# Kernel optimization log

Hardware: AMD Instinct MI355X
Metric: run time of the kernel (lower is better)

Reference implementation:

```python
import jax, jax.numpy as jnp
import numpy as np

N = 65536   # total goals in library
D = 256     # flattened embedding dim
B = 2048    # batch_size (last B entries are the new batch)


def setup_inputs() -> dict:
    key = jax.random.key(0)
    k1, k2 = jax.random.split(key)
    return {
        "target_lib": jax.random.normal(k1, (N, D), dtype=jnp.float32),
        "reached_lib": jax.random.normal(k2, (N, D), dtype=jnp.float32),
        "batch_size": B,
    }


def _euclid(a, b):
    # distance_fn: Euclidean distance between two embeddings
    return jnp.sqrt(jnp.sum((a - b) ** 2))


def _nearest_idx(queries, lib):
    # top-1 nearest neighbor via squared-distance expansion (same argmin as cdist)
    qn = jnp.sum(queries * queries, axis=1, keepdims=True)      # [B,1]
    ln = jnp.sum(lib * lib, axis=1)                             # [L]
    d2 = qn + ln[None, :] - 2.0 * (queries @ lib.T)             # [B,L]
    return jnp.argmin(d2, axis=1)                               # [B]


def reference(target_lib, reached_lib, batch_size):
    targets = target_lib[-batch_size:]          # [B,D] newest target goals
    reached = reached_lib[-batch_size:]         # [B,D] newest reached goals
    prev = reached_lib[:-batch_size]            # [N-B,D] previously reached goals

    prev_closest = prev[_nearest_idx(targets, prev)]       # [B,D]
    new_closest = reached[_nearest_idx(targets, reached)]  # [B,D]

    def LP(t, init_e, reached_e):
        return _euclid(t, init_e) - _euclid(t, reached_e)

    IM_vals, IM_grads = jax.vmap(jax.value_and_grad(LP, 0))(
        targets, prev_closest, new_closest)
    return IM_vals, IM_grads
```

## Files before the change

### kernel.cpp

```cpp
#include <hip/hip_runtime.h>
#include <math.h>

#define NTOT   65536
#define DDIM   256
#define BATCH  2048
#define NPREV  (NTOT - BATCH)

#define NC_P 31
#define CHUNK_P 2048
#define NC_R 16
#define CHUNK_R 128

#define INF_F 3.402823466e+38f
#define SWZ(r) ((((r) & 3)) ^ ((((r) >> 2) & 3)))

typedef float  f32x4  __attribute__((ext_vector_type(4)));
typedef float  f32x16 __attribute__((ext_vector_type(16)));
typedef _Float16 half8 __attribute__((ext_vector_type(8)));

#define TILE_HALVES 65536
#define KB_HALVES   8192

#define SCHED_FENCE() __builtin_amdgcn_sched_barrier(0)
#define RAW_BARRIER() do { SCHED_FENCE(); __builtin_amdgcn_s_barrier(); SCHED_FENCE(); } while (0)
#define VMCNT8()  do { asm volatile("s_waitcnt vmcnt(8)" ::: "memory"); SCHED_FENCE(); } while (0)
#define VMCNT0()  do { asm volatile("s_waitcnt vmcnt(0)" ::: "memory"); SCHED_FENCE(); } while (0)

__global__ void lp_norms(const float* __restrict__ lib, float* __restrict__ ln) {
    const int row  = blockIdx.x * 4 + (threadIdx.x >> 6);
    const int lane = threadIdx.x & 63;
    const float4 v = reinterpret_cast<const float4*>(lib + (size_t)row * DDIM)[lane];
    float s = v.x * v.x + v.y * v.y + v.z * v.z + v.w * v.w;
#pragma unroll
    for (int off = 32; off > 0; off >>= 1) s += __shfl_down(s, off);
    if (lane == 0) ln[row] = s;
}

__device__ __forceinline__ void cvt_split(const f32x4 a, const f32x4 b,
                                          half8& h, half8& l) {
    float v[8] = {a[0], a[1], a[2], a[3], b[0], b[1], b[2], b[3]};
#pragma unroll
    for (int j = 0; j < 8; ++j) {
        const float s = v[j] * 256.0f;
        const _Float16 hh = (_Float16)s;
        const _Float16 ll = (_Float16)(s - (float)hh);
        h[j] = hh; l[j] = ll;
    }
}

__global__ void lp_split32(const float* __restrict__ src, _Float16* __restrict__ dst,
                           float* __restrict__ ln) {
    const int tile = blockIdx.x;
    const int t    = threadIdx.x;
    const int rg   = t >> 6;
    const int l    = t & 63;
    const int row  = rg * 32 + (l & 31);
    const int k8   = l >> 5;
    const float* srcR = src + (size_t)tile * 128 * DDIM + (size_t)row * DDIM;
    _Float16*    dstT = dst + (size_t)tile * TILE_HALVES;

    float nsum = 0.f;
#pragma unroll
    for (int kb = 0; kb < 8; ++kb) {
#pragma unroll
        for (int kk = 0; kk < 2; ++kk) {
            const float* p = srcR + kb * 32 + kk * 16 + k8 * 8;
            const f32x4 a = *reinterpret_cast<const f32x4*>(p);
            const f32x4 b = *reinterpret_cast<const f32x4*>(p + 4);
            half8 h, lo; cvt_split(a, b, h, lo);
            const size_t off = ((size_t)(((kb * 2 + 0) * 4 + rg) * 2 + kk) * 64 + l) * 8;
            *reinterpret_cast<half8*>(dstT + off)        = h;
            *reinterpret_cast<half8*>(dstT + off + 4096) = lo;
            nsum += a[0]*a[0] + a[1]*a[1] + a[2]*a[2] + a[3]*a[3]
                  + b[0]*b[0] + b[1]*b[1] + b[2]*b[2] + b[3]*b[3];
        }
    }
    nsum += __shfl_xor(nsum, 32);
    if (ln != nullptr && k8 == 0) ln[(size_t)tile * 128 + row] = nsum;
}

__device__ __forceinline__ void stage4k(_Float16* lds, const _Float16* g, int t) {
    const int wid = t >> 6;
    __builtin_amdgcn_global_load_lds(
        (const __attribute__((address_space(1))) void*)(g + (size_t)t * 8),
        (__attribute__((address_space(3))) void*)(lds + (size_t)wid * 512),
        16, 0, 0);
}

__global__ __launch_bounds__(256, 2)
void lp_nn_mfma5(const _Float16* __restrict__ Qs, const _Float16* __restrict__ Ls,
                 const float* __restrict__ ln, int chunkRows,
                 float* __restrict__ pscore, int* __restrict__ pidx, int nchunks)
{
    __shared__ _Float16 B0[16384];
    __shared__ _Float16 B1[16384];
    __shared__ float xk[2][128];
    __shared__ int   xi[2][128];

    const int nwg  = 16 * nchunks;
    const int hid  = blockIdx.x;
    const int work = (hid & 7) * (nwg >> 3) + (hid >> 3);
    const int bx   = work & 15;
    const int by   = work >> 4;

    const int t    = threadIdx.x;
    const int wid  = t >> 6, lane = t & 63;
    const int wq   = wid >> 1, wl = wid & 1;
    const int col  = lane & 31, hi = lane >> 5;
    const int chunkBase = by * chunkRows;

    const _Float16* Qtile = Qs + (size_t)bx * TILE_HALVES;
    const _Float16* Lbase = Ls + (size_t)(chunkBase >> 7) * TILE_HALVES;
    const int NSTEP = (chunkRows >> 7) * 8;

    float bkey[2][16];
    int   bidxr[2][16];
    f32x16 acc[2][2];
#pragma unroll
    for (int mf = 0; mf < 2; ++mf) {
#pragma unroll
        for (int r = 0; r < 16; ++r) { bkey[mf][r] = INF_F; bidxr[mf][r] = 0x7fffffff; }
#pragma unroll
        for (int nf = 0; nf < 2; ++nf) acc[mf][nf] = (f32x16)(0.f);
    }

    auto stage = [&](_Float16* dst, int s) {
        const int kb = s & 7, lt = s >> 3;
        const _Float16* Qkb = Qtile + kb * KB_HALVES;
        const _Float16* Lkb = Lbase + (size_t)lt * TILE_HALVES + kb * KB_HALVES;
#pragma unroll
        for (int i = 0; i < 4; ++i) stage4k(dst + i * 2048,        Qkb + i * 2048, t);
#pragma unroll
        for (int i = 0; i < 4; ++i) stage4k(dst + 8192 + i * 2048, Lkb + i * 2048, t);
    };

    auto compute = [&](const _Float16* buf, int s) {
        const _Float16* Ab = buf;
        const _Float16* Bb = buf + 8192;
#pragma unroll
        for (int kk = 0; kk < 2; ++kk) {
            half8 a[2][2], b[2][2];
#pragma unroll
            for (int mf = 0; mf < 2; ++mf)
#pragma unroll
                for (int hl = 0; hl < 2; ++hl) {
                    a[mf][hl] = *reinterpret_cast<const half8*>(
                        Ab + (((hl * 4 + (wq * 2 + mf)) * 2 + kk) * 64 + lane) * 8);
                    b[mf][hl] = *reinterpret_cast<const half8*>(
                        Bb + (((hl * 4 + (wl * 2 + mf)) * 2 + kk) * 64 + lane) * 8);
                }
#pragma unroll
            for (int nf = 0; nf < 2; ++nf)
#pragma unroll
                for (int mf = 0; mf < 2; ++mf) {
                    acc[mf][nf] = __builtin_amdgcn_mfma_f32_32x32x16_f16(a[mf][0], b[nf][0], acc[mf][nf], 0, 0, 0);
                    acc[mf][nf] = __builtin_amdgcn_mfma_f32_32x32x16_f16(a[mf][0], b[nf][1], acc[mf][nf], 0, 0, 0);
                    acc[mf][nf] = __builtin_amdgcn_mfma_f32_32x32x16_f16(a[mf][1], b[nf][0], acc[mf][nf], 0, 0, 0);
                }
        }
        if ((s & 7) == 7) {
            const int ltbase = chunkBase + ((s >> 3) << 7);
#pragma unroll
            for (int nf = 0; nf < 2; ++nf) {
                const int gidx = ltbase + wl * 64 + nf * 32 + col;
                const float lnv = ln[gidx] * 65536.0f;
#pragma unroll
                for (int mf = 0; mf < 2; ++mf)
#pragma unroll
                    for (int r = 0; r < 16; ++r) {
                        const float key = fmaf(-2.f, acc[mf][nf][r], lnv);
                        if (key < bkey[mf][r] || (key == bkey[mf][r] && gidx < bidxr[mf][r])) {
                            bkey[mf][r] = key; bidxr[mf][r] = gidx;
                        }
                        acc[mf][nf][r] = 0.f;
                    }
            }
        }
    };

    stage(B0, 0);
    for (int s = 0; s < NSTEP; s += 2) {
        stage(B1, s + 1);
        VMCNT8();
        RAW_BARRIER();
        compute(B0, s);
        RAW_BARRIER();
        if (s + 2 < NSTEP) { stage(B0, s + 2); VMCNT8(); }
        else               { VMCNT0(); }
        RAW_BARRIER();
        compute(B1, s + 1);
        RAW_BARRIER();
    }

#pragma unroll
    for (int off = 1; off < 32; off <<= 1) {
#pragma unroll
        for (int mf = 0; mf < 2; ++mf)
#pragma unroll
            for (int r = 0; r < 16; ++r) {
                const float ok = __shfl_xor(bkey[mf][r], off);
                const int   oi = __shfl_xor(bidxr[mf][r], off);
                if (ok < bkey[mf][r] || (ok == bkey[mf][r] && oi < bidxr[mf][r])) {
                    bkey[mf][r] = ok; bidxr[mf][r] = oi;
                }
            }
    }
    if (col == 0) {
#pragma unroll
        for (int mf = 0; mf < 2; ++mf)
#pragma unroll
            for (int r = 0; r < 16; ++r) {
                const int ql = wq * 64 + mf * 32 + (r & 3) + 8 * (r >> 2) + 4 * hi;
                xk[wl][ql] = bkey[mf][r];
                xi[wl][ql] = bidxr[mf][r];
            }
    }
    __syncthreads();
    if (t < 128) {
        float bk = xk[0][t]; int bi = xi[0][t];
        const float k2 = xk[1][t]; const int i2 = xi[1][t];
        if (k2 < bk || (k2 == bk && i2 < bi)) { bk = k2; bi = i2; }
        const int q = bx * 128 + t;
        pscore[(size_t)q * nchunks + by] = bk;
        pidx  [(size_t)q * nchunks + by] = bi;
    }
}

__global__ __launch_bounds__(256, 2)
void lp_nn_mfma_fb(const float* __restrict__ Q, const float* __restrict__ L,
                   const float* __restrict__ ln, int chunkRows,
                   float* __restrict__ pscore, int* __restrict__ pidx, int nchunks)
{
    __shared__ _Float16 Ah[128 * 32];
    __shared__ _Float16 Al[128 * 32];
    __shared__ _Float16 Bh[128 * 32];
    __shared__ _Float16 Bl[128 * 32];
    __shared__ float xk[2][128];
    __shared__ int   xi[2][128];

    const int t    = threadIdx.x;
    const int wid  = t >> 6, lane = t & 63;
    const int wq   = wid >> 1, wl = wid & 1;
    const int col  = lane & 15, rg = lane >> 4;
    const int qbase = blockIdx.x * 128;
    const int chunkBase = blockIdx.y * chunkRows;
    const int srow   = t >> 2;
    const int schunk = t & 3;

    float bkey[4][4];
    int   bidxr[4][4];
#pragma unroll
    for (int mf = 0; mf < 4; ++mf)
#pragma unroll
        for (int i = 0; i < 4; ++i) { bkey[mf][i] = INF_F; bidxr[mf][i] = 0x7fffffff; }

    for (int lt = 0; lt < chunkRows; lt += 128) {
        f32x4 acc[4][4];
#pragma unroll
        for (int mf = 0; mf < 4; ++mf)
#pragma unroll
            for (int nf = 0; nf < 4; ++nf) acc[mf][nf] = (f32x4)(0.f);

        for (int kb = 0; kb < DDIM; kb += 32) {
            __syncthreads();
#pragma unroll
            for (int sr = 0; sr < 2; ++sr) {
                const int r = srow + 64 * sr;
                const int s = schunk ^ SWZ(r);
                {
                    const float* src = Q + (size_t)(qbase + r) * DDIM + kb + schunk * 8;
                    const f32x4 a = *reinterpret_cast<const f32x4*>(src);
                    const f32x4 b = *reinterpret_cast<const f32x4*>(src + 4);
                    half8 h, l; cvt_split(a, b, h, l);
                    *reinterpret_cast<half8*>(&Ah[r * 32 + s * 8]) = h;
                    *reinterpret_cast<half8*>(&Al[r * 32 + s * 8]) = l;
                }
                {
                    const float* src = L + (size_t)(chunkBase + lt + r) * DDIM + kb + schunk * 8;
                    const f32x4 a = *reinterpret_cast<const f32x4*>(src);
                    const f32x4 b = *reinterpret_cast<const f32x4*>(src + 4);
                    half8 h, l; cvt_split(a, b, h, l);
                    *reinterpret_cast<half8*>(&Bh[r * 32 + s * 8]) = h;
                    *reinterpret_cast<half8*>(&Bl[r * 32 + s * 8]) = l;
                }
            }
            __syncthreads();

            half8 ah[4], al[4];
#pragma unroll
            for (int mf = 0; mf < 4; ++mf) {
                const int r = wq * 64 + mf * 16 + col;
                const int s = rg ^ SWZ(r);
                ah[mf] = *reinterpret_cast<const half8*>(&Ah[r * 32 + s * 8]);
                al[mf] = *reinterpret_cast<const half8*>(&Al[r * 32 + s * 8]);
            }
#pragma unroll
            for (int nf = 0; nf < 4; ++nf) {
                const int r = wl * 64 + nf * 16 + col;
                const int s = rg ^ SWZ(r);
                const half8 bh = *reinterpret_cast<const half8*>(&Bh[r * 32 + s * 8]);
                const half8 bl = *reinterpret_cast<const half8*>(&Bl[r * 32 + s * 8]);
#pragma unroll
                for (int mf = 0; mf < 4; ++mf) {
                    acc[mf][nf] = __builtin_amdgcn_mfma_f32_16x16x32_f16(ah[mf], bh, acc[mf][nf], 0, 0, 0);
                    acc[mf][nf] = __builtin_amdgcn_mfma_f32_16x16x32_f16(ah[mf], bl, acc[mf][nf], 0, 0, 0);
                    acc[mf][nf] = __builtin_amdgcn_mfma_f32_16x16x32_f16(al[mf], bh, acc[mf][nf], 0, 0, 0);
                }
            }
        }

#pragma unroll
        for (int nf = 0; nf < 4; ++nf) {
            const int gidx = chunkBase + lt + wl * 64 + nf * 16 + col;
            const float lnv = ln[gidx] * 65536.0f;
#pragma unroll
            for (int mf = 0; mf < 4; ++mf)
#pragma unroll
                for (int i = 0; i < 4; ++i) {
                    const float key = fmaf(-2.f, acc[mf][nf][i], lnv);
                    if (key < bkey[mf][i] || (key == bkey[mf][i] && gidx < bidxr[mf][i])) {
                        bkey[mf][i] = key; bidxr[mf][i] = gidx;
                    }
                }
        }
    }

#pragma unroll
    for (int off = 1; off < 16; off <<= 1) {
#pragma unroll
        for (int mf = 0; mf < 4; ++mf)
#pragma unroll
            for (int i = 0; i < 4; ++i) {
                const float ok = __shfl_xor(bkey[mf][i], off);
                const int   oi = __shfl_xor(bidxr[mf][i], off);
                if (ok < bkey[mf][i] || (ok == bkey[mf][i] && oi < bidxr[mf][i])) {
                    bkey[mf][i] = ok; bidxr[mf][i] = oi;
                }
            }
    }
    if (col == 0) {
#pragma unroll
        for (int mf = 0; mf < 4; ++mf)
#pragma unroll
            for (int i = 0; i < 4; ++i) {
                const int ql = wq * 64 + mf * 16 + rg * 4 + i;
                xk[wl][ql] = bkey[mf][i];
                xi[wl][ql] = bidxr[mf][i];
            }
    }
    __syncthreads();
    if (t < 128) {
        float bk = xk[0][t]; int bi = xi[0][t];
        const float k2 = xk[1][t]; const int i2 = xi[1][t];
        if (k2 < bk || (k2 == bk && i2 < bi)) { bk = k2; bi = i2; }
        const int q = qbase + t;
        pscore[(size_t)q * nchunks + blockIdx.y] = bk;
        pidx  [(size_t)q * nchunks + blockIdx.y] = bi;
    }
}

__global__ void lp_finalize(const float* __restrict__ Q,
                            const float* __restrict__ prevL,
                            const float* __restrict__ reachL,
                            const float* __restrict__ ps_p, const int* __restrict__ pi_p,
                            const float* __restrict__ ps_r, const int* __restrict__ pi_r,
                            float* __restrict__ out)
{
    const int q = blockIdx.x;
    const int lane = threadIdx.x;

    float k1 = (lane < NC_P) ? ps_p[(size_t)q * NC_P + lane] : INF_F;
    int   i1 = (lane < NC_P) ? pi_p[(size_t)q * NC_P + lane] : 0x7fffffff;
#pragma unroll
    for (int off = 32; off > 0; off >>= 1) {
        const float ok = __shfl_xor(k1, off);
        const int   oi = __shfl_xor(i1, off);
        if (ok < k1 || (ok == k1 && oi < i1)) { k1 = ok; i1 = oi; }
    }
    float k2 = (lane < NC_R) ? ps_r[(size_t)q * NC_R + lane] : INF_F;
    int   i2 = (lane < NC_R) ? pi_r[(size_t)q * NC_R + lane] : 0x7fffffff;
#pragma unroll
    for (int off = 32; off > 0; off >>= 1) {
        const float ok = __shfl_xor(k2, off);
        const int   oi = __shfl_xor(i2, off);
        if (ok < k2 || (ok == k2 && oi < i2)) { k2 = ok; i2 = oi; }
    }

    const float4 tv = reinterpret_cast<const float4*>(Q      + (size_t)q  * DDIM)[lane];
    const float4 e1 = reinterpret_cast<const float4*>(prevL  + (size_t)i1 * DDIM)[lane];
    const float4 e2 = reinterpret_cast<const float4*>(reachL + (size_t)i2 * DDIM)[lane];
    const float4 d1 = {tv.x - e1.x, tv.y - e1.y, tv.z - e1.z, tv.w - e1.w};
    const float4 d2 = {tv.x - e2.x, tv.y - e2.y, tv.z - e2.z, tv.w - e2.w};
    float s1 = d1.x * d1.x + d1.y * d1.y + d1.z * d1.z + d1.w * d1.w;
    float s2 = d2.x * d2.x + d2.y * d2.y + d2.z * d2.z + d2.w * d2.w;
#pragma unroll
    for (int off = 32; off > 0; off >>= 1) {
        s1 += __shfl_xor(s1, off);
        s2 += __shfl_xor(s2, off);
    }
    const float r1 = sqrtf(s1), r2 = sqrtf(s2);
    float4 g;
    g.x = d1.x / r1 - d2.x / r2;
    g.y = d1.y / r1 - d2.y / r2;
    g.z = d1.z / r1 - d2.z / r2;
    g.w = d1.w / r1 - d2.w / r2;
    reinterpret_cast<float4*>(out + BATCH + (size_t)q * DDIM)[lane] = g;
    if (lane == 0) out[q] = r1 - r2;
}

extern "C" void kernel_launch(void* const* d_in, const int* in_sizes, int n_in,
                              void* d_out, int out_size, void* d_ws, size_t ws_size,
                              hipStream_t stream) {
    const float* target_lib  = (const float*)d_in[0];
    const float* reached_lib = (const float*)d_in[1];
    const float* Qp     = target_lib  + (size_t)NPREV * DDIM;
    const float* prevL  = reached_lib;
    const float* reachL = reached_lib + (size_t)NPREV * DDIM;

    float* ws     = (float*)d_ws;
    float* ln_all = ws;
    float* ps_p   = ln_all + NTOT;
    float* ps_r   = ps_p + (size_t)BATCH * NC_P;
    int*   pi_p   = (int*)(ps_r + (size_t)BATCH * NC_R);
    int*   pi_r   = pi_p + (size_t)BATCH * NC_P;
    _Float16* Qsp = (_Float16*)(pi_r + (size_t)BATCH * NC_R);
    _Float16* Lsp = Qsp + (size_t)(BATCH / 128) * TILE_HALVES;
    float* out    = (float*)d_out;

    const size_t need = 1032192u
                      + (size_t)(BATCH / 128) * TILE_HALVES * 2
                      + (size_t)(NTOT / 128) * TILE_HALVES * 2;

    if (ws_size >= need) {
        lp_split32<<<NTOT / 128, 256, 0, stream>>>(reached_lib, Lsp, ln_all);
        lp_split32<<<BATCH / 128, 256, 0, stream>>>(Qp, Qsp, nullptr);
        lp_nn_mfma5<<<16 * NC_P, 256, 0, stream>>>(
            Qsp, Lsp, ln_all, CHUNK_P, ps_p, pi_p, NC_P);
        lp_nn_mfma5<<<16 * NC_R, 256, 0, stream>>>(
            Qsp, Lsp + (size_t)(NPREV / 128) * TILE_HALVES,
            ln_all + NPREV, CHUNK_R, ps_r, pi_r, NC_R);
    } else {
        lp_norms<<<NTOT / 4, 256, 0, stream>>>(reached_lib, ln_all);
        lp_nn_mfma_fb<<<dim3(BATCH / 128, NC_P), 256, 0, stream>>>(
            Qp, prevL, ln_all, CHUNK_P, ps_p, pi_p, NC_P);
        lp_nn_mfma_fb<<<dim3(BATCH / 128, NC_R), 256, 0, stream>>>(
            Qp, reachL, ln_all + NPREV, CHUNK_R, ps_r, pi_r, NC_R);
    }
    lp_finalize<<<BATCH, 64, 0, stream>>>(Qp, prevL, reachL, ps_p, pi_p, ps_r, pi_r, out);
}
```

Measured before the change: 278.5 us.

## Widen NN kernel to 256-query tiles with 8 waves and staged norms

Replaces the 256-thread 128x128 MFMA nearest-neighbor kernel with a 512-thread variant in which each workgroup covers 256 queries against 128 library rows per step. Library tiles are now reused across twice as many queries. Library norms are preloaded into LDS, and the next stage is issued after compute within each step. LDS fragment loads are split around the MFMA groups with barriers and setprio hints. The reached-chunk split changes to 8 chunks of 256 rows. The cost is more LDS per workgroup and more barriers per step, which may reduce occupancy.

```diff
diff --git a/kernel.cpp b/kernel.cpp
--- a/kernel.cpp
+++ b/kernel.cpp
@@ -8,8 +8,8 @@
 
 #define NC_P 31
 #define CHUNK_P 2048
-#define NC_R 16
-#define CHUNK_R 128
+#define NC_R 8
+#define CHUNK_R 256
 
 #define INF_F 3.402823466e+38f
 #define SWZ(r) ((((r) & 3)) ^ ((((r) >> 2) & 3)))
@@ -23,8 +23,9 @@
 
 #define SCHED_FENCE() __builtin_amdgcn_sched_barrier(0)
 #define RAW_BARRIER() do { SCHED_FENCE(); __builtin_amdgcn_s_barrier(); SCHED_FENCE(); } while (0)
-#define VMCNT8()  do { asm volatile("s_waitcnt vmcnt(8)" ::: "memory"); SCHED_FENCE(); } while (0)
+#define VMCNT6()  do { asm volatile("s_waitcnt vmcnt(6)" ::: "memory"); SCHED_FENCE(); } while (0)
 #define VMCNT0()  do { asm volatile("s_waitcnt vmcnt(0)" ::: "memory"); SCHED_FENCE(); } while (0)
+#define LGKM0()   do { asm volatile("s_waitcnt lgkmcnt(0)" ::: "memory"); SCHED_FENCE(); } while (0)
 
 __global__ void lp_norms(const float* __restrict__ lib, float* __restrict__ ln) {
     const int row  = blockIdx.x * 4 + (threadIdx.x >> 6);
@@ -79,39 +80,51 @@
     if (ln != nullptr && k8 == 0) ln[(size_t)tile * 128 + row] = nsum;
 }
 
-__device__ __forceinline__ void stage4k(_Float16* lds, const _Float16* g, int t) {
-    const int wid = t >> 6;
+__device__ __forceinline__ void stage8(_Float16* lds, const _Float16* g, int t) {
     __builtin_amdgcn_global_load_lds(
         (const __attribute__((address_space(1))) void*)(g + (size_t)t * 8),
-        (__attribute__((address_space(3))) void*)(lds + (size_t)wid * 512),
+        (__attribute__((address_space(3))) void*)(lds + (size_t)(t >> 6) * 512),
         16, 0, 0);
 }
 
-__global__ __launch_bounds__(256, 2)
-void lp_nn_mfma5(const _Float16* __restrict__ Qs, const _Float16* __restrict__ Ls,
+__global__ __launch_bounds__(512, 2)
+void lp_nn_mfma6(const _Float16* __restrict__ Qs, const _Float16* __restrict__ Ls,
                  const float* __restrict__ ln, int chunkRows,
                  float* __restrict__ pscore, int* __restrict__ pidx, int nchunks)
 {
-    __shared__ _Float16 B0[16384];
-    __shared__ _Float16 B1[16384];
-    __shared__ float xk[2][128];
-    __shared__ int   xi[2][128];
-
-    const int nwg  = 16 * nchunks;
+    __shared__ _Float16 B0[24576];
+    __shared__ _Float16 B1[24576];
+    __shared__ float lnLds[2048];
+    __shared__ float xk[2][256];
+    __shared__ int   xi[2][256];
+
+    const int nwg  = 8 * nchunks;
     const int hid  = blockIdx.x;
     const int work = (hid & 7) * (nwg >> 3) + (hid >> 3);
-    const int bx   = work & 15;
-    const int by   = work >> 4;
+    const int bx   = work & 7;
+    const int by   = work >> 3;
 
     const int t    = threadIdx.x;
-    const int wid  = t >> 6, lane = t & 63;
-    const int wq   = wid >> 1, wl = wid & 1;
+    const int lane = t & 63;
+    const int wid  = t >> 6;
+    const int wq   = wid >> 1;
+    const int wl   = wid & 1;
     const int col  = lane & 31, hi = lane >> 5;
     const int chunkBase = by * chunkRows;
 
-    const _Float16* Qtile = Qs + (size_t)bx * TILE_HALVES;
+    const _Float16* Qt    = Qs + (size_t)(bx * 2) * TILE_HALVES;
     const _Float16* Lbase = Ls + (size_t)(chunkBase >> 7) * TILE_HALVES;
     const int NSTEP = (chunkRows >> 7) * 8;
+
+    int aB[2], bB[2];
+#pragma unroll
+    for (int mf = 0; mf < 2; ++mf) {
+        const int ql = wq * 64 + mf * 32;
+        aB[mf] = (ql >> 7) * 8192 + ((ql >> 5) & 3) * 1024 + lane * 8;
+    }
+#pragma unroll
+    for (int nf = 0; nf < 2; ++nf)
+        bB[nf] = 16384 + (wl * 2 + nf) * 1024 + lane * 8;
 
     float bkey[2][16];
     int   bidxr[2][16];
@@ -126,74 +139,90 @@
 
     auto stage = [&](_Float16* dst, int s) {
         const int kb = s & 7, lt = s >> 3;
-        const _Float16* Qkb = Qtile + kb * KB_HALVES;
+        const _Float16* Q0  = Qt + kb * KB_HALVES;
+        const _Float16* Q1  = Qt + TILE_HALVES + kb * KB_HALVES;
         const _Float16* Lkb = Lbase + (size_t)lt * TILE_HALVES + kb * KB_HALVES;
-#pragma unroll
-        for (int i = 0; i < 4; ++i) stage4k(dst + i * 2048,        Qkb + i * 2048, t);
-#pragma unroll
-        for (int i = 0; i < 4; ++i) stage4k(dst + 8192 + i * 2048, Lkb + i * 2048, t);
+        stage8(dst + 0,     Q0 + 0,    t);
+        stage8(dst + 4096,  Q0 + 4096, t);
+        stage8(dst + 8192,  Q1 + 0,    t);
+        stage8(dst + 12288, Q1 + 4096, t);
+        stage8(dst + 16384, Lkb + 0,    t);
+        stage8(dst + 20480, Lkb + 4096, t);
     };
 
-    auto compute = [&](const _Float16* buf, int s) {
-        const _Float16* Ab = buf;
-        const _Float16* Bb = buf + 8192;
-#pragma unroll
-        for (int kk = 0; kk < 2; ++kk) {
-            half8 a[2][2], b[2][2];
+    auto fold = [&](int lt) {
+#pragma unroll
+        for (int nf = 0; nf < 2; ++nf) {
+            const int lrow = lt * 128 + wl * 64 + nf * 32 + col;
+            const float lnv = lnLds[lrow] * 65536.0f;
+            const int gidx = chunkBase + lrow;
 #pragma unroll
             for (int mf = 0; mf < 2; ++mf)
 #pragma unroll
-                for (int hl = 0; hl < 2; ++hl) {
-                    a[mf][hl] = *reinterpret_cast<const half8*>(
-                        Ab + (((hl * 4 + (wq * 2 + mf)) * 2 + kk) * 64 + lane) * 8);
-                    b[mf][hl] = *reinterpret_cast<const half8*>(
-                        Bb + (((hl * 4 + (wl * 2 + mf)) * 2 + kk) * 64 + lane) * 8);
-                }
-#pragma unroll
-            for (int nf = 0; nf < 2; ++nf)
-#pragma unroll
-                for (int mf = 0; mf < 2; ++mf) {
-                    acc[mf][nf] = __builtin_amdgcn_mfma_f32_32x32x16_f16(a[mf][0], b[nf][0], acc[mf][nf], 0, 0, 0);
-                    acc[mf][nf] = __builtin_amdgcn_mfma_f32_32x32x16_f16(a[mf][0], b[nf][1], acc[mf][nf], 0, 0, 0);
-                    acc[mf][nf] = __builtin_amdgcn_mfma_f32_32x32x16_f16(a[mf][1], b[nf][0], acc[mf][nf], 0, 0, 0);
-                }
-        }
-        if ((s & 7) == 7) {
-            const int ltbase = chunkBase + ((s >> 3) << 7);
-#pragma unroll
-            for (int nf = 0; nf < 2; ++nf) {
-                const int gidx = ltbase + wl * 64 + nf * 32 + col;
-                const float lnv = ln[gidx] * 65536.0f;
-#pragma unroll
-                for (int mf = 0; mf < 2; ++mf)
-#pragma unroll
-                    for (int r = 0; r < 16; ++r) {
-                        const float key = fmaf(-2.f, acc[mf][nf][r], lnv);
-                        if (key < bkey[mf][r] || (key == bkey[mf][r] && gidx < bidxr[mf][r])) {
-                            bkey[mf][r] = key; bidxr[mf][r] = gidx;
-                        }
-                        acc[mf][nf][r] = 0.f;
+                for (int r = 0; r < 16; ++r) {
+                    const float key = fmaf(-2.f, acc[mf][nf][r], lnv);
+                    if (key < bkey[mf][r] || (key == bkey[mf][r] && gidx < bidxr[mf][r])) {
+                        bkey[mf][r] = key; bidxr[mf][r] = gidx;
                     }
-            }
+                    acc[mf][nf][r] = 0.f;
+                }
         }
     };
 
+    auto step = [&](_Float16* buf, int s) {
+        if (s + 1 < NSTEP) VMCNT6(); else VMCNT0();
+        RAW_BARRIER();
+        half8 a[2][2], bb[2];
+#pragma unroll
+        for (int kk = 0; kk < 2; ++kk) {
+#pragma unroll
+            for (int mf = 0; mf < 2; ++mf)
+#pragma unroll
+                for (int hl = 0; hl < 2; ++hl)
+                    a[mf][hl] = *reinterpret_cast<const half8*>(buf + aB[mf] + hl * 4096 + kk * 512);
+#pragma unroll
+            for (int hl = 0; hl < 2; ++hl)
+                bb[hl] = *reinterpret_cast<const half8*>(buf + bB[0] + hl * 4096 + kk * 512);
+            RAW_BARRIER(); LGKM0();
+            __builtin_amdgcn_s_setprio(1);
+#pragma unroll
+            for (int mf = 0; mf < 2; ++mf) {
+                acc[mf][0] = __builtin_amdgcn_mfma_f32_32x32x16_f16(a[mf][0], bb[0], acc[mf][0], 0, 0, 0);
+                acc[mf][0] = __builtin_amdgcn_mfma_f32_32x32x16_f16(a[mf][0], bb[1], acc[mf][0], 0, 0, 0);
+                acc[mf][0] = __builtin_amdgcn_mfma_f32_32x32x16_f16(a[mf][1], bb[0], acc[mf][0], 0, 0, 0);
+            }
+            __builtin_amdgcn_s_setprio(0);
+#pragma unroll
+            for (int hl = 0; hl < 2; ++hl)
+                bb[hl] = *reinterpret_cast<const half8*>(buf + bB[1] + hl * 4096 + kk * 512);
+            RAW_BARRIER(); LGKM0();
+            __builtin_amdgcn_s_setprio(1);
+#pragma unroll
+            for (int mf = 0; mf < 2; ++mf) {
+                acc[mf][1] = __builtin_amdgcn_mfma_f32_32x32x16_f16(a[mf][0], bb[0], acc[mf][1], 0, 0, 0);
+                acc[mf][1] = __builtin_amdgcn_mfma_f32_32x32x16_f16(a[mf][0], bb[1], acc[mf][1], 0, 0, 0);
+                acc[mf][1] = __builtin_amdgcn_mfma_f32_32x32x16_f16(a[mf][1], bb[0], acc[mf][1], 0, 0, 0);
+            }
+            __builtin_amdgcn_s_setprio(0);
+        }
+        RAW_BARRIER();
+        if (s + 2 < NSTEP) stage(buf, s + 2);
+        if ((s & 7) == 7) fold(s >> 3);
+    };
+
+    for (int i = t; i < chunkRows; i += 512) lnLds[i] = ln[chunkBase + i];
+    SCHED_FENCE();
     stage(B0, 0);
+    stage(B1, 1);
+    LGKM0();
+
     for (int s = 0; s < NSTEP; s += 2) {
-        stage(B1, s + 1);
-        VMCNT8();
-        RAW_BARRIER();
-        compute(B0, s);
-        RAW_BARRIER();
-        if (s + 2 < NSTEP) { stage(B0, s + 2); VMCNT8(); }
-        else               { VMCNT0(); }
-        RAW_BARRIER();
-        compute(B1, s + 1);
-        RAW_BARRIER();
-    }
-
-#pragma unroll
-    for (int off = 1; off < 32; off <<= 1) {
+        step(B0, s);
+        step(B1, s + 1);
+    }
+
+#pragma unroll
+    for (int off = 1; off < 32; off <<= 1)
 #pragma unroll
         for (int mf = 0; mf < 2; ++mf)
 #pragma unroll
@@ -204,8 +233,7 @@
                     bkey[mf][r] = ok; bidxr[mf][r] = oi;
                 }
             }
-    }
-    if (col == 0) {
+    if (col == 0)
 #pragma unroll
         for (int mf = 0; mf < 2; ++mf)
 #pragma unroll
@@ -214,13 +242,12 @@
                 xk[wl][ql] = bkey[mf][r];
                 xi[wl][ql] = bidxr[mf][r];
             }
-    }
     __syncthreads();
-    if (t < 128) {
+    if (t < 256) {
         float bk = xk[0][t]; int bi = xi[0][t];
         const float k2 = xk[1][t]; const int i2 = xi[1][t];
         if (k2 < bk || (k2 == bk && i2 < bi)) { bk = k2; bi = i2; }
-        const int q = bx * 128 + t;
+        const int q = bx * 256 + t;
         pscore[(size_t)q * nchunks + by] = bk;
         pidx  [(size_t)q * nchunks + by] = bi;
     }
@@ -326,7 +353,7 @@
     }
 
 #pragma unroll
-    for (int off = 1; off < 16; off <<= 1) {
+    for (int off = 1; off < 16; off <<= 1)
 #pragma unroll
         for (int mf = 0; mf < 4; ++mf)
 #pragma unroll
@@ -337,8 +364,7 @@
                     bkey[mf][i] = ok; bidxr[mf][i] = oi;
                 }
             }
-    }
-    if (col == 0) {
+    if (col == 0)
 #pragma unroll
         for (int mf = 0; mf < 4; ++mf)
 #pragma unroll
@@ -347,7 +373,6 @@
                 xk[wl][ql] = bkey[mf][i];
                 xi[wl][ql] = bidxr[mf][i];
             }
-    }
     __syncthreads();
     if (t < 128) {
         float bk = xk[0][t]; int bi = xi[0][t];
@@ -427,16 +452,15 @@
     _Float16* Lsp = Qsp + (size_t)(BATCH / 128) * TILE_HALVES;
     float* out    = (float*)d_out;
 
-    const size_t need = 1032192u
-                      + (size_t)(BATCH / 128) * TILE_HALVES * 2
-                      + (size_t)(NTOT / 128) * TILE_HALVES * 2;
+    const size_t need = (size_t)(NTOT + 2 * BATCH * (NC_P + NC_R)) * 4
+                      + (size_t)(BATCH / 128 + NTOT / 128) * TILE_HALVES * 2;
 
     if (ws_size >= need) {
         lp_split32<<<NTOT / 128, 256, 0, stream>>>(reached_lib, Lsp, ln_all);
         lp_split32<<<BATCH / 128, 256, 0, stream>>>(Qp, Qsp, nullptr);
-        lp_nn_mfma5<<<16 * NC_P, 256, 0, stream>>>(
+        lp_nn_mfma6<<<8 * NC_P, 512, 0, stream>>>(
             Qsp, Lsp, ln_all, CHUNK_P, ps_p, pi_p, NC_P);
-        lp_nn_mfma5<<<16 * NC_R, 256, 0, stream>>>(
+        lp_nn_mfma6<<<8 * NC_R, 512, 0, stream>>>(
             Qsp, Lsp + (size_t)(NPREV / 128) * TILE_HALVES,
             ln_all + NPREV, CHUNK_R, ps_r, pi_r, NC_R);
     } else {
```

New measurement: 301.2 us. 8.2% more time.
